# Optimization experiments

Measured on AMD Instinct MI355X. Metric: run time of the kernel, lower is better.

## Reference

```python
import jax, jax.numpy as jnp
import numpy as np

WD = 7                      # width == height == 7 (hard-coded 6/7 constants in source)
SCALE = 0.3
NUM_CLASSES = 17
IN_FEAT = NUM_CLASSES * 10 * WD * WD  # 8330
BS = 4096
GROUPS = [("head", 2), ("arm", 2), ("upper", 2), ("lower", 2), ("foot", 1)]
KEY_IDX = {"head": [0, 1, 3, 4], "arm": [7, 8, 9, 10], "upper": [5, 6, 11, 12],
           "lower": [11, 12, 13, 14], "foot": [15, 16]}


def setup_inputs() -> dict:
    key = jax.random.key(0)
    ks = jax.random.split(key, 2 + 2 * len(GROUPS))
    inp = {
        "x": jax.random.normal(ks[0], (BS, IN_FEAT), jnp.float32),
        "keypoint": jax.random.uniform(ks[1], (BS, 17, 2), jnp.float32),
    }
    i = 2
    for name, g in GROUPS:
        inp[f"W_{name}"] = jax.random.normal(ks[i], (IN_FEAT, g * 2 * WD), jnp.float32) * 0.01
        inp[f"b_{name}"] = jax.random.normal(ks[i + 1], (g * 2 * WD,), jnp.float32) * 0.01
        i += 2
    return inp


def _gen_map(vec, kp):
    """vec: (bs, G, 2, WD) float; kp: (bs, K, 2) int32. Returns (bs, G, 1, WD, WD)."""
    v = jnp.exp(jax.nn.softmax(vec, axis=2))  # softmax over the size-2 axis, then exp
    cols = jnp.arange(WD)

    def cum(a, keep):  # masked normalize + cumsum; a: (bs,G,WD), keep: (bs,1,WD) bool
        am = jnp.where(keep, a, 0.0)
        return jnp.cumsum(am / am.sum(-1, keepdims=True), axis=-1)

    def axis_mask(a, k):  # a: (bs,G,WD), k: (bs,K) int
        lo = jnp.maximum(k.min(axis=1) - 1, 0)[:, None, None]          # zero cols < lo
        hi = jnp.minimum(k.max(axis=1) + 1, WD - 1)[:, None, None]      # zero cols >= hi
        c1 = cum(a, cols >= lo)
        c1 = jnp.where(c1 >= SCALE, c1, 0.0)
        c2 = 1.0 - cum(a, cols < hi)
        c2 = jnp.where(c2 >= SCALE, c2, 0.0)
        return c1 * c2

    xm = axis_mask(v[:, :, 0], kp[:, :, 0])   # (bs,G,WD)
    ym = axis_mask(v[:, :, 1], kp[:, :, 1])   # (bs,G,WD)
    m = ym[:, :, :, None] * xm[:, :, None, :]  # (bs,G,WD,WD): rows=y, cols=x
    # per-sample global max over (G,WD,WD); .item() in torch detaches it
    mx = jax.lax.stop_gradient(m.max(axis=(1, 2, 3), keepdims=True))
    m = m / (mx + 1e-7)
    return m[:, :, None]  # (bs, G, 1, WD, WD)


def reference(x, keypoint, W_head, b_head, W_arm, b_arm, W_upper, b_upper,
              W_lower, b_lower, W_foot, b_foot):
    bs = x.shape[0]
    kp = jnp.minimum(jnp.floor(keypoint * 7.0).astype(jnp.int32), 6)  # (bs,17,2)
    params = {"head": (W_head, b_head), "arm": (W_arm, b_arm),
              "upper": (W_upper, b_upper), "lower": (W_lower, b_lower),
              "foot": (W_foot, b_foot)}
    outs = []
    for name, _ in GROUPS:
        W, b = params[name]
        vec = (x @ W + b).reshape(bs, -1, 2, WD)            # (bs,G,2,WD)
        outs.append(_gen_map(vec, kp[:, jnp.array(KEY_IDX[name])]))
    return tuple(outs)
```

## Files before the change

### kernel.cpp

```cpp
#include <hip/hip_runtime.h>

typedef _Float16 half8 __attribute__((ext_vector_type(8)));
typedef float f32x4 __attribute__((ext_vector_type(4)));

#define WD 7
#define NPAD 128
#define KDIM 8330
#define BSZ 4096
#define SPLITK 8
#define NTILES 261
#define BM 64
#define BK 32

static constexpr size_t OFF_WT   = 0;
static constexpr size_t WT_BYTES = (size_t)NTILES * 16384;
static constexpr size_t OFF_BIAS = WT_BYTES;
static constexpr size_t OFF_PART = OFF_BIAS + 512;

static __device__ const int KIDX[5][4] = {
    {0, 1, 3, 4}, {7, 8, 9, 10}, {5, 6, 11, 12}, {11, 12, 13, 14}, {15, 16, 15, 16}};
static __device__ const unsigned long long OBASE[5] = {0ull, 401408ull, 802816ull, 1204224ull, 1605632ull};

__device__ __forceinline__ int tile0_of(int s) { return 33 * s - max(0, s - 5); }
__device__ __forceinline__ int niter_of(int s) { return (s < 5) ? 33 : 32; }

__device__ __forceinline__ unsigned pk16(_Float16 a, _Float16 b) {
  return (unsigned)__builtin_bit_cast(unsigned short, a) |
         ((unsigned)__builtin_bit_cast(unsigned short, b) << 16);
}

__device__ __forceinline__ void gload_lds4(const void* g, void* l) {
  __builtin_amdgcn_global_load_lds((const __attribute__((address_space(1))) unsigned int*)g,
                                   (__attribute__((address_space(3))) unsigned int*)l, 4, 0, 0);
}
__device__ __forceinline__ void gload_lds16(const void* g, void* l) {
  __builtin_amdgcn_global_load_lds((const __attribute__((address_space(1))) unsigned int*)g,
                                   (__attribute__((address_space(3))) unsigned int*)l, 16, 0, 0);
}

__global__ __launch_bounds__(256) void pack_kernel(
    const float* __restrict__ Wh, const float* __restrict__ bh,
    const float* __restrict__ Wa, const float* __restrict__ ba,
    const float* __restrict__ Wu, const float* __restrict__ bu,
    const float* __restrict__ Wl_, const float* __restrict__ bl,
    const float* __restrict__ Wf, const float* __restrict__ bf,
    char* __restrict__ wsb) {
  _Float16* wt = (_Float16*)(wsb + OFF_WT);
  float* bias = (float*)(wsb + OFF_BIAS);
  __shared__ _Float16 sh[64][128];
  __shared__ _Float16 sl[64][128];
  const int k0 = blockIdx.x * 64;
  const int tid = threadIdx.x;

#pragma unroll
  for (int jj = 0; jj < 32; ++jj) {
    int idx = tid + 256 * jj;
    int kk = idx >> 7, n = idx & 127;
    int k = k0 + kk;
    float w = 0.f;
    if (k < KDIM) {
      if      (n < 28)  w = Wh [k * 28 + n];
      else if (n < 56)  w = Wa [k * 28 + (n - 28)];
      else if (n < 84)  w = Wu [k * 28 + (n - 56)];
      else if (n < 112) w = Wl_[k * 28 + (n - 84)];
      else if (n < 126) w = Wf [k * 14 + (n - 112)];
    }
    _Float16 h = (_Float16)w;
    _Float16 l = (_Float16)((w - (float)h) * 2048.0f);
    sh[kk][n] = h;
    sl[kk][n] = l;
  }
  if (blockIdx.x == 0 && tid < NPAD) {
    int n = tid;
    float v = 0.f;
    if      (n < 28)  v = bh[n];
    else if (n < 56)  v = ba[n - 28];
    else if (n < 84)  v = bu[n - 56];
    else if (n < 112) v = bl[n - 84];
    else if (n < 126) v = bf[n - 112];
    bias[n] = v;
  }
  __syncthreads();
  const int n = tid >> 1;
  const int kc = (tid & 1) * 32;
  const int kglob = k0 + kc;
  if (kglob < NTILES * 32) {
    const int tile = kglob >> 5;
    _Float16* tb = wt + (size_t)tile * 8192;
#pragma unroll
    for (int c = 0; c < 4; ++c) {
      int sp = c ^ ((n >> 1) & 3);
      uint4 qh, ql;
      qh.x = pk16(sh[kc + c * 8 + 0][n], sh[kc + c * 8 + 1][n]);
      qh.y = pk16(sh[kc + c * 8 + 2][n], sh[kc + c * 8 + 3][n]);
      qh.z = pk16(sh[kc + c * 8 + 4][n], sh[kc + c * 8 + 5][n]);
      qh.w = pk16(sh[kc + c * 8 + 6][n], sh[kc + c * 8 + 7][n]);
      ql.x = pk16(sl[kc + c * 8 + 0][n], sl[kc + c * 8 + 1][n]);
      ql.y = pk16(sl[kc + c * 8 + 2][n], sl[kc + c * 8 + 3][n]);
      ql.z = pk16(sl[kc + c * 8 + 4][n], sl[kc + c * 8 + 5][n]);
      ql.w = pk16(sl[kc + c * 8 + 6][n], sl[kc + c * 8 + 7][n]);
      *(uint4*)(tb + (size_t)n * 32 + sp * 8)        = qh;
      *(uint4*)(tb + 4096 + (size_t)n * 32 + sp * 8) = ql;
    }
  }
}

__global__ __launch_bounds__(256) void gemm_kernel(const float* __restrict__ x,
                                                   char* __restrict__ wsb) {
  const _Float16* wt = (const _Float16*)(wsb + OFF_WT);
  float* partial = (float*)(wsb + OFF_PART);
  const int bid = blockIdx.x;
  const int split = bid & 7;
  const int row0 = (bid >> 3) * BM;
  const int tile0 = tile0_of(split);
  const int ks = tile0 * 32;
  const int niter = niter_of(split);

  __shared__ float alds[3][64][32];
  __shared__ _Float16 wlds[2][128][32];

  const int tid = threadIdx.x;
  const int lane = tid & 63;
  const int wid = tid >> 6;
  const int wm = wid & 1;
  const int wn = wid >> 1;

  const int rowlane = lane >> 5;
  const int up = (lane >> 2) & 7;
  const int fof = lane & 3;
  const float* xsrc[8];
#pragma unroll
  for (int j = 0; j < 8; ++j) {
    int row = wid * 16 + 2 * j + rowlane;
    int koff = ((up ^ (row & 7)) << 2) + fof;
    xsrc[j] = x + (size_t)(row0 + row) * KDIM + koff;
  }
  auto stageX = [&](int buf, int kb) {
    if (kb + BK <= KDIM) {
#pragma unroll
      for (int j = 0; j < 8; ++j)
        gload_lds4((const void*)(xsrc[j] + kb), (void*)&alds[buf][wid * 16 + 2 * j][0]);
    } else {
#pragma unroll
      for (int j = 0; j < 8; ++j) {
        int row = wid * 16 + 2 * j + rowlane;
        int k = kb + ((up ^ (row & 7)) << 2) + fof;
        float v = (k < KDIM) ? x[(size_t)(row0 + row) * KDIM + k] : 0.f;
        alds[buf][row][lane & 31] = v;
      }
    }
  };

  auto stageW = [&](int tile) {
    const _Float16* src = wt + (size_t)tile * 8192 + (size_t)wid * 2048 + (size_t)lane * 8;
#pragma unroll
    for (int c = 0; c < 4; ++c) {
      int chunk = wid * 4 + c;
      gload_lds16((const void*)(src + c * 512),
                  (void*)((char*)&wlds[0][0][0] + chunk * 1024));
    }
  };

  f32x4 accA[2][4], accB[2][4];
#pragma unroll
  for (int mt = 0; mt < 2; ++mt)
#pragma unroll
    for (int nt = 0; nt < 4; ++nt) { accA[mt][nt] = (f32x4)(0.f); accB[mt][nt] = (f32x4)(0.f); }

  const int fr = lane & 15;
  const int fslot = lane >> 4;

  stageW(tile0);
  stageX(0, ks);
  stageX(1, ks + BK);
  asm volatile("s_waitcnt vmcnt(8) lgkmcnt(0)" ::: "memory");
  __builtin_amdgcn_s_barrier();

  int xbuf = 0;
  for (int t = 0; t < niter; ++t) {
    float4 fa[2], fb[2];
    half8 b_h[4], b_l[4];
#pragma unroll
    for (int mt = 0; mt < 2; ++mt) {
      int row = wm * 32 + mt * 16 + fr;
      int u0 = (2 * fslot) ^ (row & 7);
      int u1 = (2 * fslot + 1) ^ (row & 7);
      fa[mt] = *(const float4*)&alds[xbuf][row][u0 * 4];
      fb[mt] = *(const float4*)&alds[xbuf][row][u1 * 4];
    }
#pragma unroll
    for (int nt = 0; nt < 4; ++nt) {
      int col = wn * 64 + nt * 16 + fr;
      int sp = fslot ^ ((col >> 1) & 3);
      b_h[nt] = *(const half8*)&wlds[0][col][sp * 8];
      b_l[nt] = *(const half8*)&wlds[1][col][sp * 8];
    }
    asm volatile("s_waitcnt lgkmcnt(0)" ::: "memory");
    __builtin_amdgcn_s_barrier();

    if (t + 1 < niter) stageW(tile0 + t + 1);
    if (t + 2 < niter) {
      int nb = xbuf + 2; if (nb >= 3) nb -= 3;
      stageX(nb, ks + (t + 2) * BK);
    }
    __builtin_amdgcn_sched_barrier(0);

    half8 a_h[2], a_l[2];
#pragma unroll
    for (int mt = 0; mt < 2; ++mt) {
      float fv[8] = {fa[mt].x, fa[mt].y, fa[mt].z, fa[mt].w,
                     fb[mt].x, fb[mt].y, fb[mt].z, fb[mt].w};
#pragma unroll
      for (int i = 0; i < 8; ++i) {
        _Float16 h = (_Float16)fv[i];
        a_h[mt][i] = h;
        a_l[mt][i] = (_Float16)((fv[i] - (float)h) * 2048.0f);
      }
    }
    __builtin_amdgcn_s_setprio(1);
#pragma unroll
    for (int mt = 0; mt < 2; ++mt)
#pragma unroll
      for (int nt = 0; nt < 4; ++nt) {
        accA[mt][nt] = __builtin_amdgcn_mfma_f32_16x16x32_f16(a_h[mt], b_h[nt], accA[mt][nt], 0, 0, 0);
        accB[mt][nt] = __builtin_amdgcn_mfma_f32_16x16x32_f16(a_l[mt], b_h[nt], accB[mt][nt], 0, 0, 0);
        accB[mt][nt] = __builtin_amdgcn_mfma_f32_16x16x32_f16(a_h[mt], b_l[nt], accB[mt][nt], 0, 0, 0);
      }
    __builtin_amdgcn_s_setprio(0);

    if (t + 1 < niter) {
      if (t + 2 < niter)
        asm volatile("s_waitcnt vmcnt(8) lgkmcnt(0)" ::: "memory");
      else
        asm volatile("s_waitcnt vmcnt(0) lgkmcnt(0)" ::: "memory");
      __builtin_amdgcn_s_barrier();
    }
    ++xbuf; if (xbuf >= 3) xbuf = 0;
  }

  float* pb = partial + (size_t)split * BSZ * NPAD;
#pragma unroll
  for (int mt = 0; mt < 2; ++mt)
#pragma unroll
    for (int nt = 0; nt < 4; ++nt) {
      int col = wn * 64 + nt * 16 + fr;
#pragma unroll
      for (int r = 0; r < 4; ++r) {
        int row = row0 + wm * 32 + mt * 16 + fslot * 4 + r;
        pb[(size_t)row * NPAD + col] = accA[mt][nt][r] + accB[mt][nt][r] * (1.0f / 2048.0f);
      }
    }
}

__device__ __forceinline__ void axis_mask(const float a[WD], int lo, int hi, float m[WD]) {
  float am[WD];
  float tot = 0.f;
#pragma unroll
  for (int c = 0; c < WD; ++c) { am[c] = (c >= lo) ? a[c] : 0.f; tot += am[c]; }
  float run = 0.f;
  float c1[WD];
#pragma unroll
  for (int c = 0; c < WD; ++c) {
    run += am[c] / tot;
    c1[c] = (run >= 0.3f) ? run : 0.f;
  }
  float tot2 = 0.f;
#pragma unroll
  for (int c = 0; c < WD; ++c) { am[c] = (c < hi) ? a[c] : 0.f; tot2 += am[c]; }
  run = 0.f;
#pragma unroll
  for (int c = 0; c < WD; ++c) {
    run += am[c] / tot2;
    float c2 = 1.f - run;
    c2 = (c2 >= 0.3f) ? c2 : 0.f;
    m[c] = c1[c] * c2;
  }
}

__global__ __launch_bounds__(256) void epi_kernel(const char* __restrict__ wsb,
                                                  const float* __restrict__ keypoint,
                                                  float* __restrict__ out) {
  __shared__ float vlds[16][132];
  const int b0 = blockIdx.x * 16;
  const int tid = threadIdx.x;
  const float4* part4 = (const float4*)(wsb + OFF_PART);
  const float4* bias4 = (const float4*)(wsb + OFF_BIAS);

  float4 a[2];
#pragma unroll
  for (int j = 0; j < 2; ++j) {
    int fi = tid * 2 + j;
    a[j] = part4[((size_t)(b0 + (fi >> 5))) * 32 + (fi & 31)];
  }
  for (int sp = 1; sp < SPLITK; ++sp) {
#pragma unroll
    for (int j = 0; j < 2; ++j) {
      int fi = tid * 2 + j;
      float4 p = part4[((size_t)sp * BSZ + b0 + (fi >> 5)) * 32 + (fi & 31)];
      a[j].x += p.x; a[j].y += p.y; a[j].z += p.z; a[j].w += p.w;
    }
  }
#pragma unroll
  for (int j = 0; j < 2; ++j) {
    int fi = tid * 2 + j;
    float4 bb = bias4[fi & 31];
    a[j].x += bb.x; a[j].y += bb.y; a[j].z += bb.z; a[j].w += bb.w;
    *(float4*)&vlds[fi >> 5][(fi & 31) * 4] = a[j];
  }
  __syncthreads();

  if (tid < 80) {
    int fam = tid >> 4;
    int bl = tid & 15;
    int b = b0 + bl;
    const int G = (fam == 4) ? 1 : 2;
    const int nk = (fam == 4) ? 2 : 4;
    const float* vv = &vlds[bl][fam * 28];

    int mnx = 7, mxx = -1, mny = 7, mxy = -1;
    for (int i = 0; i < nk; ++i) {
      int kidx = KIDX[fam][i];
      float fx = keypoint[((size_t)b * 17 + kidx) * 2 + 0];
      float fy = keypoint[((size_t)b * 17 + kidx) * 2 + 1];
      int ix = (int)floorf(fx * 7.0f); ix = ix < 6 ? ix : 6;
      int iy = (int)floorf(fy * 7.0f); iy = iy < 6 ? iy : 6;
      mnx = min(mnx, ix); mxx = max(mxx, ix);
      mny = min(mny, iy); mxy = max(mxy, iy);
    }
    int lox = mnx - 1; if (lox < 0) lox = 0;
    int hix = mxx + 1; if (hix > 6) hix = 6;
    int loy = mny - 1; if (loy < 0) loy = 0;
    int hiy = mxy + 1; if (hiy > 6) hiy = 6;

    float xmg[2][WD], ymg[2][WD];
    float mx = 0.f;
#pragma unroll
    for (int g = 0; g < 2; ++g) {
      if (g < G) {
        const float* vg = vv + g * 14;
        float a0[WD], a1[WD];
#pragma unroll
        for (int c = 0; c < WD; ++c) {
          float s0 = vg[c], s1 = vg[c + 7];
          float mM = fmaxf(s0, s1);
          float e0 = expf(s0 - mM), e1 = expf(s1 - mM);
          float sum = e0 + e1;
          a0[c] = expf(e0 / sum);
          a1[c] = expf(e1 / sum);
        }
        axis_mask(a0, lox, hix, xmg[g]);
        axis_mask(a1, loy, hiy, ymg[g]);
        float mx_x = 0.f, mx_y = 0.f;
#pragma unroll
        for (int c = 0; c < WD; ++c) {
          mx_x = fmaxf(mx_x, xmg[g][c]);
          mx_y = fmaxf(mx_y, ymg[g][c]);
        }
        mx = fmaxf(mx, mx_y * mx_x);
      }
    }

    float d = mx + 1e-7f;
    float* op = out + OBASE[fam] + (size_t)b * (G * 49);
#pragma unroll
    for (int g = 0; g < 2; ++g) {
      if (g < G) {
#pragma unroll
        for (int y = 0; y < WD; ++y) {
          float yv = ymg[g][y];
#pragma unroll
          for (int xx = 0; xx < WD; ++xx) {
            op[g * 49 + y * 7 + xx] = (yv * xmg[g][xx]) / d;
          }
        }
      }
    }
  }
}

extern "C" void kernel_launch(void* const* d_in, const int* in_sizes, int n_in,
                              void* d_out, int out_size, void* d_ws, size_t ws_size,
                              hipStream_t stream) {
  const float* x        = (const float*)d_in[0];
  const float* keypoint = (const float*)d_in[1];
  const float* Wh = (const float*)d_in[2];
  const float* bh = (const float*)d_in[3];
  const float* Wa = (const float*)d_in[4];
  const float* ba = (const float*)d_in[5];
  const float* Wu = (const float*)d_in[6];
  const float* bu = (const float*)d_in[7];
  const float* Wl = (const float*)d_in[8];
  const float* bl = (const float*)d_in[9];
  const float* Wf = (const float*)d_in[10];
  const float* bf = (const float*)d_in[11];
  float* out = (float*)d_out;
  char* wsb  = (char*)d_ws;

  const int packBlocks = (NTILES * 32 + 63) / 64;
  hipLaunchKernelGGL(pack_kernel, dim3(packBlocks), dim3(256), 0, stream,
                     Wh, bh, Wa, ba, Wu, bu, Wl, bl, Wf, bf, wsb);
  hipLaunchKernelGGL(gemm_kernel, dim3((BSZ / BM) * SPLITK), dim3(256), 0, stream, x, wsb);
  hipLaunchKernelGGL(epi_kernel, dim3(BSZ / 16), dim3(256), 0, stream,
                     wsb, keypoint, out);
}
```

Before: 71.59 us.

## Double the split-K factor and restructure GEMM pipeline to double-buffered W and X

Raises the split-K factor from 8 to 16, so each block covers half as many K tiles and the grid holds twice as many blocks. The old three-stage X buffer and single W buffer with mid-loop barriers become a two-stage double buffer for both operands, with a single wait-all plus barrier at the top of each iteration. B fragments are now loaded from LDS inside the MFMA loop, and launch bounds request three blocks per SM. The intent is more parallelism and occupancy to hide load latency. In exchange, twice as many partial sums must be written and reduced, and waiting on all outstanding loads each iteration may expose memory latency. This also assumes the partial buffer and the reduce kernel handle 16 splits.

```diff
diff --git a/kernel.cpp b/kernel.cpp
--- a/kernel.cpp
+++ b/kernel.cpp
@@ -7,7 +7,7 @@
 #define NPAD 128
 #define KDIM 8330
 #define BSZ 4096
-#define SPLITK 8
+#define SPLITK 16
 #define NTILES 261
 #define BM 64
 #define BK 32
@@ -21,8 +21,8 @@
     {0, 1, 3, 4}, {7, 8, 9, 10}, {5, 6, 11, 12}, {11, 12, 13, 14}, {15, 16, 15, 16}};
 static __device__ const unsigned long long OBASE[5] = {0ull, 401408ull, 802816ull, 1204224ull, 1605632ull};
 
-__device__ __forceinline__ int tile0_of(int s) { return 33 * s - max(0, s - 5); }
-__device__ __forceinline__ int niter_of(int s) { return (s < 5) ? 33 : 32; }
+__device__ __forceinline__ int tile0_of(int s) { return 16 * s + min(s, 5); }
+__device__ __forceinline__ int niter_of(int s) { return (s < 5) ? 17 : 16; }
 
 __device__ __forceinline__ unsigned pk16(_Float16 a, _Float16 b) {
   return (unsigned)__builtin_bit_cast(unsigned short, a) |
@@ -105,19 +105,19 @@
   }
 }
 
-__global__ __launch_bounds__(256) void gemm_kernel(const float* __restrict__ x,
-                                                   char* __restrict__ wsb) {
+__global__ __launch_bounds__(256, 3) void gemm_kernel(const float* __restrict__ x,
+                                                      char* __restrict__ wsb) {
   const _Float16* wt = (const _Float16*)(wsb + OFF_WT);
   float* partial = (float*)(wsb + OFF_PART);
   const int bid = blockIdx.x;
-  const int split = bid & 7;
-  const int row0 = (bid >> 3) * BM;
+  const int split = bid & 15;
+  const int row0 = (bid >> 4) * BM;
   const int tile0 = tile0_of(split);
   const int ks = tile0 * 32;
   const int niter = niter_of(split);
 
-  __shared__ float alds[3][64][32];
-  __shared__ _Float16 wlds[2][128][32];
+  __shared__ float alds[2][64][32];
+  __shared__ _Float16 wlds[2][2][128][32];
 
   const int tid = threadIdx.x;
   const int lane = tid & 63;
@@ -151,13 +151,13 @@
     }
   };
 
-  auto stageW = [&](int tile) {
+  auto stageW = [&](int buf, int tile) {
     const _Float16* src = wt + (size_t)tile * 8192 + (size_t)wid * 2048 + (size_t)lane * 8;
 #pragma unroll
     for (int c = 0; c < 4; ++c) {
       int chunk = wid * 4 + c;
       gload_lds16((const void*)(src + c * 512),
-                  (void*)((char*)&wlds[0][0][0] + chunk * 1024));
+                  (void*)((char*)&wlds[buf][0][0][0] + chunk * 1024));
     }
   };
 
@@ -170,41 +170,28 @@
   const int fr = lane & 15;
   const int fslot = lane >> 4;
 
-  stageW(tile0);
+  stageW(0, tile0);
   stageX(0, ks);
-  stageX(1, ks + BK);
-  asm volatile("s_waitcnt vmcnt(8) lgkmcnt(0)" ::: "memory");
-  __builtin_amdgcn_s_barrier();
-
-  int xbuf = 0;
+
   for (int t = 0; t < niter; ++t) {
+    const int cur = t & 1;
+    asm volatile("s_waitcnt vmcnt(0) lgkmcnt(0)" ::: "memory");
+    __builtin_amdgcn_s_barrier();
+    if (t + 1 < niter) {
+      stageW(cur ^ 1, tile0 + t + 1);
+      stageX(cur ^ 1, ks + (t + 1) * BK);
+    }
+    __builtin_amdgcn_sched_barrier(0);
+
     float4 fa[2], fb[2];
-    half8 b_h[4], b_l[4];
 #pragma unroll
     for (int mt = 0; mt < 2; ++mt) {
       int row = wm * 32 + mt * 16 + fr;
       int u0 = (2 * fslot) ^ (row & 7);
       int u1 = (2 * fslot + 1) ^ (row & 7);
-      fa[mt] = *(const float4*)&alds[xbuf][row][u0 * 4];
-      fb[mt] = *(const float4*)&alds[xbuf][row][u1 * 4];
-    }
-#pragma unroll
-    for (int nt = 0; nt < 4; ++nt) {
-      int col = wn * 64 + nt * 16 + fr;
-      int sp = fslot ^ ((col >> 1) & 3);
-      b_h[nt] = *(const half8*)&wlds[0][col][sp * 8];
-      b_l[nt] = *(const half8*)&wlds[1][col][sp * 8];
-    }
-    asm volatile("s_waitcnt lgkmcnt(0)" ::: "memory");
-    __builtin_amdgcn_s_barrier();
-
-    if (t + 1 < niter) stageW(tile0 + t + 1);
-    if (t + 2 < niter) {
-      int nb = xbuf + 2; if (nb >= 3) nb -= 3;
-      stageX(nb, ks + (t + 2) * BK);
-    }
-    __builtin_amdgcn_sched_barrier(0);
-
+      fa[mt] = *(const float4*)&alds[cur][row][u0 * 4];
+      fb[mt] = *(const float4*)&alds[cur][row][u1 * 4];
+    }
     half8 a_h[2], a_l[2];
 #pragma unroll
     for (int mt = 0; mt < 2; ++mt) {
@@ -219,23 +206,19 @@
     }
     __builtin_amdgcn_s_setprio(1);
 #pragma unroll
-    for (int mt = 0; mt < 2; ++mt)
-#pragma unroll
-      for (int nt = 0; nt < 4; ++nt) {
-        accA[mt][nt] = __builtin_amdgcn_mfma_f32_16x16x32_f16(a_h[mt], b_h[nt], accA[mt][nt], 0, 0, 0);
-        accB[mt][nt] = __builtin_amdgcn_mfma_f32_16x16x32_f16(a_l[mt], b_h[nt], accB[mt][nt], 0, 0, 0);
-        accB[mt][nt] = __builtin_amdgcn_mfma_f32_16x16x32_f16(a_h[mt], b_l[nt], accB[mt][nt], 0, 0, 0);
-      }
+    for (int nt = 0; nt < 4; ++nt) {
+      int col = wn * 64 + nt * 16 + fr;
+      int sp = fslot ^ ((col >> 1) & 3);
+      half8 b_h = *(const half8*)&wlds[cur][0][col][sp * 8];
+      half8 b_l = *(const half8*)&wlds[cur][1][col][sp * 8];
+#pragma unroll
+      for (int mt = 0; mt < 2; ++mt) {
+        accA[mt][nt] = __builtin_amdgcn_mfma_f32_16x16x32_f16(a_h[mt], b_h, accA[mt][nt], 0, 0, 0);
+        accB[mt][nt] = __builtin_amdgcn_mfma_f32_16x16x32_f16(a_l[mt], b_h, accB[mt][nt], 0, 0, 0);
+        accB[mt][nt] = __builtin_amdgcn_mfma_f32_16x16x32_f16(a_h[mt], b_l, accB[mt][nt], 0, 0, 0);
+      }
+    }
     __builtin_amdgcn_s_setprio(0);
-
-    if (t + 1 < niter) {
-      if (t + 2 < niter)
-        asm volatile("s_waitcnt vmcnt(8) lgkmcnt(0)" ::: "memory");
-      else
-        asm volatile("s_waitcnt vmcnt(0) lgkmcnt(0)" ::: "memory");
-      __builtin_amdgcn_s_barrier();
-    }
-    ++xbuf; if (xbuf >= 3) xbuf = 0;
   }
 
   float* pb = partial + (size_t)split * BSZ * NPAD;
```

After: 80.55 us. 12.5% more time.

## Switch GEMM to 32x32x16 MFMA and double-buffer the weight tile in LDS

Applied to the files above, without the earlier changes.

Replaces the 16x16x32 f16 MFMA tiling with 32x32x16 MFMAs, so each wave issues fewer, larger matrix instructions and reads fewer LDS fragments per K step. It also double-buffers the weight LDS tile, prefetching two tiles ahead to match the activation pipeline, and adjusts the vmcnt waits to cover the extra in-flight loads. This trades more LDS usage and larger accumulator register blocks for better MFMA efficiency and more load latency hiding. The output write-back index mapping is rewritten for the 32x32 accumulator layout.

```diff
diff --git a/kernel.cpp b/kernel.cpp
--- a/kernel.cpp
+++ b/kernel.cpp
@@ -1,7 +1,7 @@
 #include <hip/hip_runtime.h>
 
 typedef _Float16 half8 __attribute__((ext_vector_type(8)));
-typedef float f32x4 __attribute__((ext_vector_type(4)));
+typedef float f32x16 __attribute__((ext_vector_type(16)));
 
 #define WD 7
 #define NPAD 128
@@ -117,7 +117,7 @@
   const int niter = niter_of(split);
 
   __shared__ float alds[3][64][32];
-  __shared__ _Float16 wlds[2][128][32];
+  __shared__ _Float16 wlds[2][2][128][32];
 
   const int tid = threadIdx.x;
   const int lane = tid & 63;
@@ -151,86 +151,85 @@
     }
   };
 
-  auto stageW = [&](int tile) {
+  auto stageW = [&](int buf, int tile) {
     const _Float16* src = wt + (size_t)tile * 8192 + (size_t)wid * 2048 + (size_t)lane * 8;
 #pragma unroll
     for (int c = 0; c < 4; ++c) {
       int chunk = wid * 4 + c;
       gload_lds16((const void*)(src + c * 512),
-                  (void*)((char*)&wlds[0][0][0] + chunk * 1024));
+                  (void*)((char*)&wlds[buf][0][0][0] + chunk * 1024));
     }
   };
 
-  f32x4 accA[2][4], accB[2][4];
-#pragma unroll
-  for (int mt = 0; mt < 2; ++mt)
-#pragma unroll
-    for (int nt = 0; nt < 4; ++nt) { accA[mt][nt] = (f32x4)(0.f); accB[mt][nt] = (f32x4)(0.f); }
-
-  const int fr = lane & 15;
-  const int fslot = lane >> 4;
-
-  stageW(tile0);
+  f32x16 accA[2], accB[2];
+#pragma unroll
+  for (int nt = 0; nt < 2; ++nt) { accA[nt] = (f32x16)(0.f); accB[nt] = (f32x16)(0.f); }
+
+  const int lr = lane & 31;
+  const int khalf = lane >> 5;
+
+  stageW(0, tile0);
   stageX(0, ks);
+  stageW(1, tile0 + 1);
   stageX(1, ks + BK);
-  asm volatile("s_waitcnt vmcnt(8) lgkmcnt(0)" ::: "memory");
+  asm volatile("s_waitcnt vmcnt(12) lgkmcnt(0)" ::: "memory");
   __builtin_amdgcn_s_barrier();
 
   int xbuf = 0;
   for (int t = 0; t < niter; ++t) {
-    float4 fa[2], fb[2];
-    half8 b_h[4], b_l[4];
-#pragma unroll
-    for (int mt = 0; mt < 2; ++mt) {
-      int row = wm * 32 + mt * 16 + fr;
-      int u0 = (2 * fslot) ^ (row & 7);
-      int u1 = (2 * fslot + 1) ^ (row & 7);
-      fa[mt] = *(const float4*)&alds[xbuf][row][u0 * 4];
-      fb[mt] = *(const float4*)&alds[xbuf][row][u1 * 4];
-    }
-#pragma unroll
-    for (int nt = 0; nt < 4; ++nt) {
-      int col = wn * 64 + nt * 16 + fr;
-      int sp = fslot ^ ((col >> 1) & 3);
-      b_h[nt] = *(const half8*)&wlds[0][col][sp * 8];
-      b_l[nt] = *(const half8*)&wlds[1][col][sp * 8];
+    const int wb = t & 1;
+    float4 fA[2], fB[2];
+    half8 b_h[2][2], b_l[2][2];
+    const int arow = wm * 32 + lr;
+#pragma unroll
+    for (int ksub = 0; ksub < 2; ++ksub) {
+      int s = 2 * ksub + khalf;
+      int u0 = (2 * s) ^ (arow & 7);
+      int u1 = (2 * s + 1) ^ (arow & 7);
+      fA[ksub] = *(const float4*)&alds[xbuf][arow][u0 * 4];
+      fB[ksub] = *(const float4*)&alds[xbuf][arow][u1 * 4];
+#pragma unroll
+      for (int nt = 0; nt < 2; ++nt) {
+        int col = wn * 64 + nt * 32 + lr;
+        int sp = s ^ ((col >> 1) & 3);
+        b_h[ksub][nt] = *(const half8*)&wlds[wb][0][col][sp * 8];
+        b_l[ksub][nt] = *(const half8*)&wlds[wb][1][col][sp * 8];
+      }
     }
     asm volatile("s_waitcnt lgkmcnt(0)" ::: "memory");
     __builtin_amdgcn_s_barrier();
 
-    if (t + 1 < niter) stageW(tile0 + t + 1);
     if (t + 2 < niter) {
+      stageW(wb, tile0 + t + 2);
       int nb = xbuf + 2; if (nb >= 3) nb -= 3;
       stageX(nb, ks + (t + 2) * BK);
     }
     __builtin_amdgcn_sched_barrier(0);
 
-    half8 a_h[2], a_l[2];
-#pragma unroll
-    for (int mt = 0; mt < 2; ++mt) {
-      float fv[8] = {fa[mt].x, fa[mt].y, fa[mt].z, fa[mt].w,
-                     fb[mt].x, fb[mt].y, fb[mt].z, fb[mt].w};
+#pragma unroll
+    for (int ksub = 0; ksub < 2; ++ksub) {
+      half8 a_h, a_l;
+      float fv[8] = {fA[ksub].x, fA[ksub].y, fA[ksub].z, fA[ksub].w,
+                     fB[ksub].x, fB[ksub].y, fB[ksub].z, fB[ksub].w};
 #pragma unroll
       for (int i = 0; i < 8; ++i) {
         _Float16 h = (_Float16)fv[i];
-        a_h[mt][i] = h;
-        a_l[mt][i] = (_Float16)((fv[i] - (float)h) * 2048.0f);
-      }
-    }
-    __builtin_amdgcn_s_setprio(1);
-#pragma unroll
-    for (int mt = 0; mt < 2; ++mt)
-#pragma unroll
-      for (int nt = 0; nt < 4; ++nt) {
-        accA[mt][nt] = __builtin_amdgcn_mfma_f32_16x16x32_f16(a_h[mt], b_h[nt], accA[mt][nt], 0, 0, 0);
-        accB[mt][nt] = __builtin_amdgcn_mfma_f32_16x16x32_f16(a_l[mt], b_h[nt], accB[mt][nt], 0, 0, 0);
-        accB[mt][nt] = __builtin_amdgcn_mfma_f32_16x16x32_f16(a_h[mt], b_l[nt], accB[mt][nt], 0, 0, 0);
-      }
-    __builtin_amdgcn_s_setprio(0);
+        a_h[i] = h;
+        a_l[i] = (_Float16)((fv[i] - (float)h) * 2048.0f);
+      }
+      __builtin_amdgcn_s_setprio(1);
+#pragma unroll
+      for (int nt = 0; nt < 2; ++nt) {
+        accA[nt] = __builtin_amdgcn_mfma_f32_32x32x16_f16(a_h, b_h[ksub][nt], accA[nt], 0, 0, 0);
+        accB[nt] = __builtin_amdgcn_mfma_f32_32x32x16_f16(a_l, b_h[ksub][nt], accB[nt], 0, 0, 0);
+        accB[nt] = __builtin_amdgcn_mfma_f32_32x32x16_f16(a_h, b_l[ksub][nt], accB[nt], 0, 0, 0);
+      }
+      __builtin_amdgcn_s_setprio(0);
+    }
 
     if (t + 1 < niter) {
       if (t + 2 < niter)
-        asm volatile("s_waitcnt vmcnt(8) lgkmcnt(0)" ::: "memory");
+        asm volatile("s_waitcnt vmcnt(12) lgkmcnt(0)" ::: "memory");
       else
         asm volatile("s_waitcnt vmcnt(0) lgkmcnt(0)" ::: "memory");
       __builtin_amdgcn_s_barrier();
@@ -240,15 +239,12 @@
 
   float* pb = partial + (size_t)split * BSZ * NPAD;
 #pragma unroll
-  for (int mt = 0; mt < 2; ++mt)
-#pragma unroll
-    for (int nt = 0; nt < 4; ++nt) {
-      int col = wn * 64 + nt * 16 + fr;
-#pragma unroll
-      for (int r = 0; r < 4; ++r) {
-        int row = row0 + wm * 32 + mt * 16 + fslot * 4 + r;
-        pb[(size_t)row * NPAD + col] = accA[mt][nt][r] + accB[mt][nt][r] * (1.0f / 2048.0f);
-      }
+  for (int nt = 0; nt < 2; ++nt)
+#pragma unroll
+    for (int r = 0; r < 16; ++r) {
+      int row = row0 + wm * 32 + (r & 3) + 8 * (r >> 2) + 4 * khalf;
+      int col = wn * 64 + nt * 32 + lr;
+      pb[(size_t)row * NPAD + col] = accA[nt][r] + accB[nt][r] * (1.0f / 2048.0f);
     }
 }
 
```

After: 74.78 us. 1.04x slower.
